# Optimization experiments

Hardware: AMD Instinct MI355X
Metric: run time of the kernel (lower is better)

## Reference

```python
import jax, jax.numpy as jnp
import numpy as np

D_STATE = 16
D_CONV = 4


def layer_norm(x, g, b, eps=1e-5):
    mu = jnp.mean(x, axis=-1, keepdims=True)
    var = jnp.mean(jnp.square(x - mu), axis=-1, keepdims=True)
    return (x - mu) * jax.lax.rsqrt(var + eps) * g + b


def silu(x):
    return x * jax.nn.sigmoid(x)


def mamba(x, in_w, conv_w, conv_b, xproj_w, dt_w, dt_b, Alog, Dp, out_w):
    # x: [B, L, d_model]; in_w: [2*di, d_model]; conv_w: [di, d_conv]
    Bsz, L, _ = x.shape
    di = Dp.shape[0]
    xz = jnp.einsum('bld,ed->ble', x, in_w)          # [B,L,2*di]
    xs, z = jnp.split(xz, 2, axis=-1)
    # causal depthwise conv over L
    xt = xs.transpose(0, 2, 1)                        # [B,di,L]
    xt = jax.lax.conv_general_dilated(
        xt, conv_w[:, None, :], (1,), [(D_CONV - 1, 0)],
        feature_group_count=di, dimension_numbers=('NCH', 'OIH', 'NCH'))
    xs = silu((xt + conv_b[None, :, None]).transpose(0, 2, 1))  # [B,L,di]
    # input-dependent dt, B, C
    dbl = jnp.einsum('bld,ed->ble', xs, xproj_w)      # [B,L,dt_rank+2*ds]
    dt_rank = dt_w.shape[1]
    dt, Bc, Cc = jnp.split(dbl, [dt_rank, dt_rank + D_STATE], axis=-1)
    dt = jax.nn.softplus(jnp.einsum('blr,dr->bld', dt, dt_w) + dt_b)  # [B,L,di]
    A = -jnp.exp(Alog)                                # [di,ds]
    dA = jnp.exp(dt[..., None] * A)                   # [B,L,di,ds]
    dBx = dt[..., None] * Bc[:, :, None, :] * xs[..., None]  # [B,L,di,ds]

    def step(h, inp):
        dA_t, dBx_t, C_t = inp                        # [B,di,ds],[B,di,ds],[B,ds]
        h = dA_t * h + dBx_t
        y = jnp.einsum('bds,bs->bd', h, C_t)
        return h, y

    h0 = jnp.zeros((Bsz, di, D_STATE), x.dtype)
    _, ys = jax.lax.scan(step, h0, (dA.transpose(1, 0, 2, 3),
                                    dBx.transpose(1, 0, 2, 3),
                                    Cc.transpose(1, 0, 2)))
    y = ys.transpose(1, 0, 2) + Dp * xs               # [B,L,di]
    y = y * silu(z)
    return jnp.einsum('bld,od->blo', y, out_w)        # [B,L,d_model]


def _make_mamba_params(key, d_model, scale=0.02):
    di = 2 * d_model
    dt_rank = (d_model + 15) // 16
    ks = jax.random.split(key, 7)
    in_w = jax.random.normal(ks[0], (2 * di, d_model), jnp.float32) * scale
    conv_w = jax.random.normal(ks[1], (di, D_CONV), jnp.float32) * scale
    conv_b = jnp.zeros((di,), jnp.float32)
    xproj_w = jax.random.normal(ks[2], (dt_rank + 2 * D_STATE, di), jnp.float32) * scale
    dt_w = jax.random.normal(ks[3], (di, dt_rank), jnp.float32) * scale
    dt_b = jax.random.uniform(ks[4], (di,), jnp.float32, -5.0, -2.0)
    Alog = jnp.log(jnp.tile(jnp.arange(1, D_STATE + 1, dtype=jnp.float32), (di, 1)))
    Dp = jnp.ones((di,), jnp.float32)
    out_w = jax.random.normal(ks[5], (d_model, di), jnp.float32) * scale
    return in_w, conv_w, conv_b, xproj_w, dt_w, dt_b, Alog, Dp, out_w


def setup_inputs() -> dict:
    key = jax.random.key(0)
    B, L, D = 4, 2048, 1024
    DFF = 4 * D
    ks = jax.random.split(key, 8)
    x = jax.random.normal(ks[0], (B, L, D), jnp.float32)
    m1 = _make_mamba_params(ks[1], D)
    m2 = _make_mamba_params(ks[2], D)
    names1 = ['m1_in_w', 'm1_conv_w', 'm1_conv_b', 'm1_xproj_w', 'm1_dt_w', 'm1_dt_b', 'm1_Alog', 'm1_D', 'm1_out_w']
    names2 = ['m2_in_w', 'm2_conv_w', 'm2_conv_b', 'm2_xproj_w', 'm2_dt_w', 'm2_dt_b', 'm2_Alog', 'm2_D', 'm2_out_w']
    inp = {'x': x}
    inp.update(dict(zip(names1, m1)))
    inp.update(dict(zip(names2, m2)))
    inp['norm_g'] = jnp.ones((D,), jnp.float32)
    inp['norm_b'] = jnp.zeros((D,), jnp.float32)
    inp['ffn_g'] = jnp.ones((D,), jnp.float32)
    inp['ffn_b'] = jnp.zeros((D,), jnp.float32)
    inp['ff1_w'] = jax.random.normal(ks[3], (DFF, D), jnp.float32) * 0.02
    inp['ff1_b'] = jnp.zeros((DFF,), jnp.float32)
    inp['ff2_w'] = jax.random.normal(ks[4], (D, DFF), jnp.float32) * 0.02
    inp['ff2_b'] = jnp.zeros((D,), jnp.float32)
    return inp


def reference(x,
              m1_in_w, m1_conv_w, m1_conv_b, m1_xproj_w, m1_dt_w, m1_dt_b, m1_Alog, m1_D, m1_out_w,
              m2_in_w, m2_conv_w, m2_conv_b, m2_xproj_w, m2_dt_w, m2_dt_b, m2_Alog, m2_D, m2_out_w,
              norm_g, norm_b, ffn_g, ffn_b, ff1_w, ff1_b, ff2_w, ff2_b):
    # BiDirectionalAddBlock (dropout/droppath = identity in eval)
    h = layer_norm(x, norm_g, norm_b)
    fwd = mamba(h, m1_in_w, m1_conv_w, m1_conv_b, m1_xproj_w, m1_dt_w, m1_dt_b, m1_Alog, m1_D, m1_out_w)
    bwd = mamba(h[:, ::-1], m2_in_w, m2_conv_w, m2_conv_b, m2_xproj_w, m2_dt_w, m2_dt_b, m2_Alog, m2_D, m2_out_w)
    block_out = jax.nn.gelu(fwd + bwd + x, approximate=False)  # note: original does NOT flip bwd back
    x = x + block_out
    # FeedForward
    hf = layer_norm(x, ffn_g, ffn_b)
    hf = jax.nn.gelu(jnp.einsum('bld,hd->blh', hf, ff1_w) + ff1_b, approximate=False)
    x = x + jnp.einsum('blh,dh->bld', hf, ff2_w) + ff2_b
    return x
```

## Files before the change

kernel.cpp:

```cpp
#include <hip/hip_runtime.h>
#include <cmath>


namespace {

using u16 = unsigned short;
using uint = unsigned int;

constexpr int kB = 4;
constexpr int kL = 2048;
constexpr int kD = 1024;
constexpr int kDI = 2048;
constexpr int kDFF = 4096;
constexpr int kDS = 16;
constexpr int kDtRank = 64;
constexpr int kNPad = 128;
constexpr int kM = kB * kL;
constexpr int kNCH = 64;

typedef short bf16x8 __attribute__((ext_vector_type(8)));
typedef float f32x4  __attribute__((ext_vector_type(4)));

__device__ __forceinline__ float bf2f(u16 u) {
  union { unsigned int i; float f; } c; c.i = ((unsigned int)u) << 16; return c.f;
}
__device__ __forceinline__ u16 f2bf(float f) {
  union { float f; unsigned int i; } c; c.f = f;
  return (u16)((c.i + 0x7FFFu + ((c.i >> 16) & 1u)) >> 16);
}
__device__ __forceinline__ float geluf(float v) {
  return 0.5f * v * (1.f + erff(v * 0.70710678118654752f));
}
__device__ __forceinline__ float softplusf(float v) {
  return (v > 0.f) ? (v + log1pf(__expf(-v))) : log1pf(__expf(v));
}
__device__ __forceinline__ float siluf(float v) {
  return v / (1.f + __expf(-v));
}
__device__ __forceinline__ float exp2_fast(float v) {
  return __builtin_amdgcn_exp2f(v);
}

__device__ __forceinline__ void async16(const u16* g, u16* l) {
  __builtin_amdgcn_global_load_lds(
      (const __attribute__((address_space(1))) uint*)g,
      (__attribute__((address_space(3))) uint*)l, 16, 0, 0);
}

__global__ __launch_bounds__(256) void ln_kernel(
    const float* __restrict__ x, const float* __restrict__ g,
    const float* __restrict__ b, u16* __restrict__ out) {
  const int row = blockIdx.x;
  const int tid = threadIdx.x;
  const float4 v = ((const float4*)(x + (size_t)row * kD))[tid];
  float s  = v.x + v.y + v.z + v.w;
  float ss = v.x * v.x + v.y * v.y + v.z * v.z + v.w * v.w;
  #pragma unroll
  for (int off = 32; off; off >>= 1) {
    s  += __shfl_xor(s, off);
    ss += __shfl_xor(ss, off);
  }
  __shared__ float ls[4], lss[4];
  const int wid = tid >> 6;
  if ((tid & 63) == 0) { ls[wid] = s; lss[wid] = ss; }
  __syncthreads();
  s  = ls[0] + ls[1] + ls[2] + ls[3];
  ss = lss[0] + lss[1] + lss[2] + lss[3];
  const float mu  = s * (1.f / kD);
  const float inv = rsqrtf(ss * (1.f / kD) - mu * mu + 1e-5f);
  const float4 gg = ((const float4*)g)[tid];
  const float4 bb = ((const float4*)b)[tid];
  ushort4 o;
  o.x = f2bf((v.x - mu) * inv * gg.x + bb.x);
  o.y = f2bf((v.y - mu) * inv * gg.y + bb.y);
  o.z = f2bf((v.z - mu) * inv * gg.z + bb.z);
  o.w = f2bf((v.w - mu) * inv * gg.w + bb.w);
  ((ushort4*)(out + (size_t)row * kD))[tid] = o;
}

__global__ __launch_bounds__(256) void combine_ln_kernel(
    const float* __restrict__ x, float* __restrict__ out,
    const float* __restrict__ g, const float* __restrict__ b,
    u16* __restrict__ h) {
  const int row = blockIdx.x;
  const int tid = threadIdx.x;
  const float4 xv = ((const float4*)(x + (size_t)row * kD))[tid];
  const float4 bv = ((const float4*)(out + (size_t)row * kD))[tid];
  float4 o;
  o.x = xv.x + geluf(bv.x + xv.x);
  o.y = xv.y + geluf(bv.y + xv.y);
  o.z = xv.z + geluf(bv.z + xv.z);
  o.w = xv.w + geluf(bv.w + xv.w);
  ((float4*)(out + (size_t)row * kD))[tid] = o;
  float s  = o.x + o.y + o.z + o.w;
  float ss = o.x * o.x + o.y * o.y + o.z * o.z + o.w * o.w;
  #pragma unroll
  for (int off = 32; off; off >>= 1) {
    s  += __shfl_xor(s, off);
    ss += __shfl_xor(ss, off);
  }
  __shared__ float ls[4], lss[4];
  const int wid = tid >> 6;
  if ((tid & 63) == 0) { ls[wid] = s; lss[wid] = ss; }
  __syncthreads();
  s  = ls[0] + ls[1] + ls[2] + ls[3];
  ss = lss[0] + lss[1] + lss[2] + lss[3];
  const float mu  = s * (1.f / kD);
  const float inv = rsqrtf(ss * (1.f / kD) - mu * mu + 1e-5f);
  const float4 gg = ((const float4*)g)[tid];
  const float4 bb = ((const float4*)b)[tid];
  ushort4 ho;
  ho.x = f2bf((o.x - mu) * inv * gg.x + bb.x);
  ho.y = f2bf((o.y - mu) * inv * gg.y + bb.y);
  ho.z = f2bf((o.z - mu) * inv * gg.z + bb.z);
  ho.w = f2bf((o.w - mu) * inv * gg.w + bb.w);
  ((ushort4*)(h + (size_t)row * kD))[tid] = ho;
}

struct KJob { const float* s; u16* d; int n4; int blk0; int xp; };
struct KJobs { KJob j[10]; };

__global__ __launch_bounds__(256) void cvt_all_kernel(KJobs J) {
  const int bi = blockIdx.x;
  #pragma unroll
  for (int k = 0; k < 10; k++) {
    const KJob job = J.j[k];
    const int nb = (job.n4 + 255) >> 8;
    if (bi >= job.blk0 && bi < job.blk0 + nb) {
      const int i = (bi - job.blk0) * 256 + threadIdx.x;
      if (i < job.n4) {
        ushort4 o = {0, 0, 0, 0};
        bool valid = true;
        if (job.xp) valid = ((i * 4) >> 11) < (kDtRank + 2 * kDS);
        if (valid) {
          const float4 v = ((const float4*)job.s)[i];
          o.x = f2bf(v.x); o.y = f2bf(v.y); o.z = f2bf(v.z); o.w = f2bf(v.w);
        }
        ((ushort4*)job.d)[i] = o;
      }
      return;
    }
  }
}

template <int TILEN, int ACT, bool BIAS, bool ACC, bool OUTBF, bool REV,
          bool AMAP, bool CMAP>
__global__ __launch_bounds__(256) void gemm_mfma(
    const u16* __restrict__ A, int lda,
    const u16* __restrict__ W, int ldw,
    void* __restrict__ Cp, int ldc, int K,
    const float* __restrict__ bias, int seg_len, int row_off) {
  constexpr int MI = (TILEN == 128) ? 4 : 2;
  constexpr int WSTR = TILEN / 32;
  __shared__ __align__(16) u16 As[128][64];
  __shared__ __align__(16) u16 Ws[TILEN][64];
  const int tid  = threadIdx.x;
  const int bm   = blockIdx.x * 128;
  const int bn   = blockIdx.y * TILEN;
  const int lane = tid & 63;
  const int wv   = tid >> 6;
  const int wm   = (TILEN == 128) ? (wv >> 1) * 64 : wv * 32;
  const int wn   = (TILEN == 128) ? (wv & 1) * 64 : 0;
  const int l15  = lane & 15;
  const int quad = lane >> 4;
  const int srow = lane >> 3;
  const int swz  = ((lane & 7) ^ srow) * 8;
  const int jx   = (l15 & 7) * 16;

  int ab = 0, all0 = bm;
  if (AMAP || CMAP) {
    ab = bm / seg_len;
    all0 = bm - ab * seg_len;
  }

  int arowv[4];
  #pragma unroll
  for (int it = 0; it < 4; it++) {
    const int rl = it * 32 + wv * 8 + srow;
    if (AMAP) {
      arowv[it] = REV ? (ab * kL + kL - 1 - row_off - all0 - rl)
                      : (ab * kL + row_off + all0 + rl);
    } else {
      arowv[it] = bm + rl;
    }
  }

  f32x4 acc[MI][4];
  #pragma unroll
  for (int i = 0; i < MI; i++)
    #pragma unroll
    for (int j = 0; j < 4; j++) acc[i][j] = (f32x4){0.f, 0.f, 0.f, 0.f};

  for (int k0 = 0; k0 < K; k0 += 64) {
    #pragma unroll
    for (int it = 0; it < 4; it++) {
      const int rl = it * 32 + wv * 8 + srow;
      async16(A + (size_t)arowv[it] * lda + k0 + swz, &As[it * 32 + wv * 8][0]);
    }
    #pragma unroll
    for (int it = 0; it < WSTR; it++) {
      const int rl = it * 32 + wv * 8 + srow;
      async16(W + (size_t)(bn + rl) * ldw + k0 + swz, &Ws[it * 32 + wv * 8][0]);
    }
    __syncthreads();
    #pragma unroll
    for (int ks = 0; ks < 64; ks += 32) {
      const int cb = ((ks >> 3) + quad) * 16;
      bf16x8 af[MI], wf[4];
      #pragma unroll
      for (int i = 0; i < MI; i++)
        af[i] = *(const bf16x8*)((const char*)&As[wm + i * 16 + l15][0] +
                                 (cb ^ jx));
      #pragma unroll
      for (int j = 0; j < 4; j++)
        wf[j] = *(const bf16x8*)((const char*)&Ws[wn + j * 16 + l15][0] +
                                 (cb ^ jx));
      #pragma unroll
      for (int i = 0; i < MI; i++)
        #pragma unroll
        for (int j = 0; j < 4; j++)
          acc[i][j] = __builtin_amdgcn_mfma_f32_16x16x32_bf16(
              af[i], wf[j], acc[i][j], 0, 0, 0);
    }
    __syncthreads();
  }

  #pragma unroll
  for (int i = 0; i < MI; i++) {
    #pragma unroll
    for (int j = 0; j < 4; j++) {
      const int col = bn + wn + j * 16 + l15;
      #pragma unroll
      for (int r = 0; r < 4; r++) {
        const int rl2 = wm + i * 16 + quad * 4 + r;
        const int crow = CMAP ? (ab * kL + row_off + all0 + rl2) : (bm + rl2);
        float v = acc[i][j][r];
        if (BIAS) v += bias[col];
        if (ACT == 1) v = softplusf(v);
        if (ACT == 2) v = geluf(v);
        if (OUTBF) {
          ((u16*)Cp)[(size_t)crow * ldc + col] = f2bf(v);
        } else {
          float* p = (float*)Cp + (size_t)crow * ldc + col;
          if (ACC) *p = *p + v; else *p = v;
        }
      }
    }
  }
}

__global__ __launch_bounds__(256) void conv_silu_kernel(
    const u16* __restrict__ xz, const float* __restrict__ w,
    const float* __restrict__ cb, u16* __restrict__ xs,
    const u16* __restrict__ tail_in, u16* __restrict__ tail_out,
    int seg_len, int row_off) {
  const int t = blockIdx.x * 256 + threadIdx.x;
  const int c = t & (kDI - 1);
  const int r = t >> 11;
  const int b = r / seg_len;
  const int ll = r - b * seg_len;
  const int tpos = row_off + ll;

  const float xv0 = bf2f(xz[(size_t)r * (2 * kDI) + c]);
  float acc = cb[c] + w[c * 4 + 3] * xv0;
  #pragma unroll
  for (int j = 1; j <= 3; j++) {
    if (tpos - j >= 0) {
      float xp;
      if (ll - j >= 0) {
        xp = bf2f(xz[(size_t)(r - j) * (2 * kDI) + c]);
      } else {
        xp = bf2f(tail_in[(b * 3 + (3 + ll - j)) * kDI + c]);
      }
      acc += w[c * 4 + 3 - j] * xp;
    }
  }
  xs[(size_t)r * kDI + c] = f2bf(siluf(acc));
  if (ll >= seg_len - 3) {
    tail_out[(b * 3 + (ll - (seg_len - 3))) * kDI + c] = f2bf(xv0);
  }
}

__global__ __launch_bounds__(256, 8) void scan_phaseA(
    const u16* __restrict__ dt, const u16* __restrict__ xs,
    const u16* __restrict__ dbl, const float* __restrict__ Alog,
    float* __restrict__ Pbuf, float* __restrict__ Hbuf,
    int Lseg, int Lc) {
  __shared__ float Bls[32][16];
  const int tid = threadIdx.x;
  const int c = blockIdx.x * 256 + tid;
  const int k = blockIdx.y;
  const int b = blockIdx.z;
  const int base = b * Lseg + k * Lc;
  for (int idx = tid; idx < Lc * 16; idx += 256) {
    const int r = idx >> 4, j = idx & 15;
    Bls[r][j] = bf2f(dbl[(size_t)(base + r) * kNPad + kDtRank + j]);
  }
  __syncthreads();
  float Ac[16], h[16];
  float dtsum = 0.f;
  #pragma unroll
  for (int s = 0; s < 16; s++) {
    Ac[s] = -__expf(Alog[c * kDS + s]) * 1.44269504088896f;
    h[s] = 0.f;
  }
  for (int r = 0; r < Lc; r++) {
    const size_t row = (size_t)(base + r);
    const float dtv = bf2f(dt[row * kDI + c]);
    const float dtx = dtv * bf2f(xs[row * kDI + c]);
    dtsum += dtv;
    const float4* Brow = (const float4*)Bls[r];
    #pragma unroll
    for (int s4 = 0; s4 < 4; s4++) {
      const float4 Bv = Brow[s4];
      const float bb[4] = {Bv.x, Bv.y, Bv.z, Bv.w};
      #pragma unroll
      for (int q = 0; q < 4; q++) {
        const int s = s4 * 4 + q;
        const float dA = exp2_fast(dtv * Ac[s]);
        h[s] = dA * h[s] + dtx * bb[q];
      }
    }
  }
  const size_t o = (((size_t)b * kNCH + k) * kDI + c) * 16;
  #pragma unroll
  for (int s4 = 0; s4 < 4; s4++) {
    *(float4*)&Pbuf[o + s4 * 4] =
        make_float4(exp2_fast(Ac[s4 * 4 + 0] * dtsum),
                    exp2_fast(Ac[s4 * 4 + 1] * dtsum),
                    exp2_fast(Ac[s4 * 4 + 2] * dtsum),
                    exp2_fast(Ac[s4 * 4 + 3] * dtsum));
    *(float4*)&Hbuf[o + s4 * 4] =
        make_float4(h[s4 * 4], h[s4 * 4 + 1], h[s4 * 4 + 2], h[s4 * 4 + 3]);
  }
}

__global__ __launch_bounds__(256) void scan_phaseB(
    float* __restrict__ Pbuf, const float* __restrict__ Hbuf,
    float* __restrict__ hstate, int first) {
  const int t = blockIdx.x * 256 + threadIdx.x;
  const int s = t & 15;
  const int c = (t >> 4) & (kDI - 1);
  const int b = t >> 15;
  float cur = first ? 0.f : hstate[t];
  for (int k = 0; k < kNCH; k++) {
    const size_t idx = (((size_t)b * kNCH + k) * kDI + c) * 16 + s;
    const float p = Pbuf[idx];
    const float hl = Hbuf[idx];
    Pbuf[idx] = cur;
    cur = p * cur + hl;
  }
  hstate[t] = cur;
}

__global__ __launch_bounds__(256, 8) void scan_phaseC(
    const u16* __restrict__ dt, u16* __restrict__ xs,
    const u16* __restrict__ dbl, const u16* __restrict__ xz,
    const float* __restrict__ Alog, const float* __restrict__ Dp,
    const float* __restrict__ Pbuf, int Lseg, int Lc) {
  __shared__ float BC[32][32];
  const int tid = threadIdx.x;
  const int c = blockIdx.x * 256 + tid;
  const int k = blockIdx.y;
  const int b = blockIdx.z;
  const int base = b * Lseg + k * Lc;
  for (int idx = tid; idx < Lc * 32; idx += 256) {
    const int r = idx >> 5, j = idx & 31;
    BC[r][j] = bf2f(dbl[(size_t)(base + r) * kNPad + kDtRank + j]);
  }
  __syncthreads();
  float Ac[16], h[16];
  const size_t o = (((size_t)b * kNCH + k) * kDI + c) * 16;
  #pragma unroll
  for (int s4 = 0; s4 < 4; s4++) {
    const float4 hv = *(const float4*)&Pbuf[o + s4 * 4];
    h[s4 * 4 + 0] = hv.x; h[s4 * 4 + 1] = hv.y;
    h[s4 * 4 + 2] = hv.z; h[s4 * 4 + 3] = hv.w;
  }
  #pragma unroll
  for (int s = 0; s < 16; s++)
    Ac[s] = -__expf(Alog[c * kDS + s]) * 1.44269504088896f;
  const float Dv = Dp[c];
  for (int r = 0; r < Lc; r++) {
    const size_t row = (size_t)(base + r);
    const float dtv = bf2f(dt[row * kDI + c]);
    const float xv = bf2f(xs[row * kDI + c]);
    const float dtx = dtv * xv;
    float y = 0.f;
    const float4* Brow = (const float4*)BC[r];
    const float4* Crow = (const float4*)&BC[r][16];
    #pragma unroll
    for (int s4 = 0; s4 < 4; s4++) {
      const float4 Bv = Brow[s4];
      const float4 Cv = Crow[s4];
      const float bb[4] = {Bv.x, Bv.y, Bv.z, Bv.w};
      const float cc[4] = {Cv.x, Cv.y, Cv.z, Cv.w};
      #pragma unroll
      for (int q = 0; q < 4; q++) {
        const int s = s4 * 4 + q;
        const float dA = exp2_fast(dtv * Ac[s]);
        h[s] = dA * h[s] + dtx * bb[q];
        y += h[s] * cc[q];
      }
    }
    const float z = bf2f(xz[row * (2 * kDI) + kDI + c]);
    xs[row * kDI + c] = f2bf((y + Dv * xv) * siluf(z));
  }
}

}

extern "C" void kernel_launch(void* const* d_in, const int* in_sizes, int n_in,
                              void* d_out, int out_size, void* d_ws,
                              size_t ws_size, hipStream_t stream) {
  const float* x = (const float*)d_in[0];
  const float* in_w[2]    = {(const float*)d_in[1],  (const float*)d_in[10]};
  const float* conv_w[2]  = {(const float*)d_in[2],  (const float*)d_in[11]};
  const float* conv_b[2]  = {(const float*)d_in[3],  (const float*)d_in[12]};
  const float* xproj_w[2] = {(const float*)d_in[4],  (const float*)d_in[13]};
  const float* dt_w[2]    = {(const float*)d_in[5],  (const float*)d_in[14]};
  const float* dt_b[2]    = {(const float*)d_in[6],  (const float*)d_in[15]};
  const float* Alog[2]    = {(const float*)d_in[7],  (const float*)d_in[16]};
  const float* Dp[2]      = {(const float*)d_in[8],  (const float*)d_in[17]};
  const float* out_w[2]   = {(const float*)d_in[9],  (const float*)d_in[18]};
  const float* norm_g = (const float*)d_in[19];
  const float* norm_b = (const float*)d_in[20];
  const float* ffn_g  = (const float*)d_in[21];
  const float* ffn_b  = (const float*)d_in[22];
  const float* ff1_w  = (const float*)d_in[23];
  const float* ff1_b  = (const float*)d_in[24];
  const float* ff2_w  = (const float*)d_in[25];
  const float* ff2_b  = (const float*)d_in[26];
  float* out = (float*)d_out;

  constexpr size_t kWCache =
      2 * ((size_t)4096 * kD + (size_t)kD * kDI + (size_t)kNPad * kDI +
           (size_t)kDI * kDtRank) * 2 +
      ((size_t)kDFF * kD + (size_t)kD * kDFF) * 2;
  auto need = [](int nseg) -> size_t {
    const size_t mseg = (size_t)kM / nseg;
    size_t sz = kWCache + 4096;
    sz += (size_t)kM * kD * 2;
    sz += mseg * 4096 * 2;
    sz += mseg * 2048 * 2;
    sz += mseg * 128 * 2;
    sz += mseg * 2048 * 2;
    sz += 2 * (size_t)kB * kNCH * kDI * kDS * 4;
    sz += (size_t)kB * kDI * kDS * 4;
    sz += 2 * (size_t)kB * 3 * kDI * 2;
    sz += 32 * 256;
    return sz;
  };
  int nseg = 1;
  while (nseg <= 16 && need(nseg) > ws_size) nseg *= 2;
  if (nseg > 16) return;
  const int Lseg = kL / nseg;
  const int Mseg = kM / nseg;
  const int Lc = Lseg / kNCH;

  char* base = (char*)d_ws;
  size_t off = 0;
  auto alloc = [&](size_t bytes) {
    char* p = base + off;
    off = (off + bytes + 255) & ~(size_t)255;
    return p;
  };
  u16* w_in[2], *w_out[2], *w_xp[2], *w_dt[2];
  for (int m = 0; m < 2; m++) {
    w_in[m]  = (u16*)alloc((size_t)4096 * kD * 2);
    w_out[m] = (u16*)alloc((size_t)kD * kDI * 2);
    w_xp[m]  = (u16*)alloc((size_t)kNPad * kDI * 2);
    w_dt[m]  = (u16*)alloc((size_t)kDI * kDtRank * 2);
  }
  u16* w_f1 = (u16*)alloc((size_t)kDFF * kD * 2);
  u16* w_f2 = (u16*)alloc((size_t)kD * kDFF * 2);
  u16*   h      = (u16*)alloc((size_t)kM * kD * 2);
  u16*   xz     = (u16*)alloc((size_t)Mseg * 4096 * 2);
  u16*   xs     = (u16*)alloc((size_t)Mseg * 2048 * 2);
  u16*   dbl    = (u16*)alloc((size_t)Mseg * 128 * 2);
  u16*   dtb    = (u16*)alloc((size_t)Mseg * 2048 * 2);
  float* Pbuf   = (float*)alloc((size_t)kB * kNCH * kDI * kDS * 4);
  float* Hbuf   = (float*)alloc((size_t)kB * kNCH * kDI * kDS * 4);
  float* hstate = (float*)alloc((size_t)kB * kDI * kDS * 4);
  u16*   tail0  = (u16*)alloc((size_t)kB * 3 * kDI * 2);
  u16*   tail1  = (u16*)alloc((size_t)kB * 3 * kDI * 2);

  {
    KJobs J;
    int b = 0, ji = 0;
    auto addjob = [&](const float* s, u16* d, int n4, int xp) {
      J.j[ji].s = s; J.j[ji].d = d; J.j[ji].n4 = n4;
      J.j[ji].blk0 = b; J.j[ji].xp = xp;
      b += (n4 + 255) >> 8;
      ji++;
    };
    for (int m = 0; m < 2; m++) {
      addjob(in_w[m],  w_in[m],  (4096 * kD) / 4, 0);
      addjob(out_w[m], w_out[m], (kD * kDI) / 4, 0);
      addjob(xproj_w[m], w_xp[m], (kNPad * kDI) / 4, 1);
      addjob(dt_w[m],  w_dt[m],  (kDI * kDtRank) / 4, 0);
    }
    addjob(ff1_w, w_f1, (kDFF * kD) / 4, 0);
    addjob(ff2_w, w_f2, (kD * kDFF) / 4, 0);
    cvt_all_kernel<<<b, 256, 0, stream>>>(J);
  }

  ln_kernel<<<kM, 256, 0, stream>>>(x, norm_g, norm_b, h);

  for (int m = 0; m < 2; m++) {
    for (int s = 0; s < nseg; s++) {
      const int l0 = s * Lseg;
      u16* tin  = (s & 1) ? tail0 : tail1;
      u16* tout = (s & 1) ? tail1 : tail0;
      if (m == 0)
        gemm_mfma<128, 0, false, false, true, false, true, false>
            <<<dim3(Mseg / 128, 4096 / 128), 256, 0, stream>>>(
                h, kD, w_in[m], kD, xz, 4096, kD, nullptr, Lseg, l0);
      else
        gemm_mfma<128, 0, false, false, true, true, true, false>
            <<<dim3(Mseg / 128, 4096 / 128), 256, 0, stream>>>(
                h, kD, w_in[m], kD, xz, 4096, kD, nullptr, Lseg, l0);
      conv_silu_kernel<<<(Mseg * kDI) / 256, 256, 0, stream>>>(
          xz, conv_w[m], conv_b[m], xs, tin, tout, Lseg, l0);
      gemm_mfma<128, 0, false, false, true, false, false, false>
          <<<dim3(Mseg / 128, 1), 256, 0, stream>>>(
              xs, kDI, w_xp[m], kDI, dbl, kNPad, kDI, nullptr, Lseg, l0);
      gemm_mfma<128, 1, true, false, true, false, false, false>
          <<<dim3(Mseg / 128, kDI / 128), 256, 0, stream>>>(
              dbl, kNPad, w_dt[m], kDtRank, dtb, kDI, kDtRank, dt_b[m],
              Lseg, l0);
      scan_phaseA<<<dim3(kDI / 256, kNCH, kB), 256, 0, stream>>>(
          dtb, xs, dbl, Alog[m], Pbuf, Hbuf, Lseg, Lc);
      scan_phaseB<<<(kB * kDI * kDS) / 256, 256, 0, stream>>>(
          Pbuf, Hbuf, hstate, (s == 0) ? 1 : 0);
      scan_phaseC<<<dim3(kDI / 256, kNCH, kB), 256, 0, stream>>>(
          dtb, xs, dbl, xz, Alog[m], Dp[m], Pbuf, Lseg, Lc);
      if (m == 0)
        gemm_mfma<64, 0, false, false, false, false, false, true>
            <<<dim3(Mseg / 128, kD / 64), 256, 0, stream>>>(
                xs, kDI, w_out[m], kDI, out, kD, kDI, nullptr, Lseg, l0);
      else
        gemm_mfma<64, 0, false, true, false, false, false, true>
            <<<dim3(Mseg / 128, kD / 64), 256, 0, stream>>>(
                xs, kDI, w_out[m], kDI, out, kD, kDI, nullptr, Lseg, l0);
    }
  }

  combine_ln_kernel<<<kM, 256, 0, stream>>>(x, out, ffn_g, ffn_b, h);

  for (int s = 0; s < nseg; s++) {
    const int r0 = s * Mseg;
    gemm_mfma<128, 2, true, false, true, false, true, false>
        <<<dim3(Mseg / 128, kDFF / 128), 256, 0, stream>>>(
            h, kD, w_f1, kD, xz, kDFF, kD, ff1_b, Mseg, r0);
    gemm_mfma<64, 0, true, true, false, false, false, true>
        <<<dim3(Mseg / 128, kD / 64), 256, 0, stream>>>(
            xz, kDFF, w_f2, kDFF, out, kD, kDFF, ff2_b, Mseg, r0);
  }
}
```

Before: 1.371 ms.

## Add triple-buffered 128x256 GEMM kernel for large projections

```diff
diff --git a/kernel.cpp b/kernel.cpp
--- a/kernel.cpp
+++ b/kernel.cpp
@@ -143,24 +143,142 @@
   }
 }
 
-template <int TILEN, int ACT, bool BIAS, bool ACC, bool OUTBF, bool REV,
-          bool AMAP, bool CMAP>
+template <int ACT, bool BIAS, bool ACC, bool OUTBF, bool REV, bool AMAP,
+          bool CMAP>
+__global__ __launch_bounds__(512) void gemm_pipe(
+    const u16* __restrict__ A, int lda,
+    const u16* __restrict__ W, int ldw,
+    void* __restrict__ Cp, int ldc, int K,
+    const float* __restrict__ bias, int seg_len, int row_off) {
+  __shared__ __align__(16) u16 Abuf[3][128][64];
+  __shared__ __align__(16) u16 Bbuf[3][256][64];
+  const int tid  = threadIdx.x;
+  const int bm   = blockIdx.x * 128;
+  const int bn   = blockIdx.y * 256;
+  const int lane = tid & 63;
+  const int w    = tid >> 6;
+  const int wr   = w >> 2;
+  const int wc   = w & 3;
+  const int l15  = lane & 15;
+  const int quad = lane >> 4;
+  const int lrow = lane >> 3;
+  const int swz  = ((lane & 7) ^ lrow) * 8;
+  const int jx   = (l15 & 7) * 16;
+
+  int ab = 0, all0 = bm;
+  if (AMAP || CMAP) { ab = bm / seg_len; all0 = bm - ab * seg_len; }
+
+  int arow[2];
+  #pragma unroll
+  for (int it = 0; it < 2; it++) {
+    const int rl = it * 64 + w * 8 + lrow;
+    arow[it] = AMAP ? (REV ? (ab * kL + kL - 1 - row_off - all0 - rl)
+                           : (ab * kL + row_off + all0 + rl))
+                    : (bm + rl);
+  }
+  int brow[4];
+  #pragma unroll
+  for (int it = 0; it < 4; it++) brow[it] = bn + it * 64 + w * 8 + lrow;
+
+  const int NT = K >> 6;
+
+  f32x4 acc[4][4];
+  #pragma unroll
+  for (int i = 0; i < 4; i++)
+    #pragma unroll
+    for (int j = 0; j < 4; j++) acc[i][j] = (f32x4){0.f, 0.f, 0.f, 0.f};
+
+  auto stage = [&](int bi, int t) {
+    const int k0 = t * 64;
+    #pragma unroll
+    for (int it = 0; it < 2; it++)
+      async16(A + (size_t)arow[it] * lda + k0 + swz,
+              &Abuf[bi][it * 64 + w * 8][0]);
+    #pragma unroll
+    for (int it = 0; it < 4; it++)
+      async16(W + (size_t)brow[it] * ldw + k0 + swz,
+              &Bbuf[bi][it * 64 + w * 8][0]);
+  };
+
+  stage(0, 0);
+  stage(1, 1);
+  asm volatile("s_waitcnt vmcnt(6)\n\ts_barrier" ::: "memory");
+
+  int cur = 0, nxt = 1, nx2 = 2;
+  #pragma unroll 1
+  for (int t = 0; t < NT; t++) {
+    if (t + 2 < NT) stage(nx2, t + 2);
+    bf16x8 af[4][2], wf[4][2];
+    #pragma unroll
+    for (int ks = 0; ks < 2; ks++) {
+      const int cb = (ks * 4 + quad) * 16;
+      #pragma unroll
+      for (int i = 0; i < 4; i++)
+        af[i][ks] = *(const bf16x8*)(
+            (const char*)&Abuf[cur][wr * 64 + i * 16 + l15][0] + (cb ^ jx));
+      #pragma unroll
+      for (int j = 0; j < 4; j++)
+        wf[j][ks] = *(const bf16x8*)(
+            (const char*)&Bbuf[cur][wc * 64 + j * 16 + l15][0] + (cb ^ jx));
+    }
+    __builtin_amdgcn_s_setprio(1);
+    #pragma unroll
+    for (int ks = 0; ks < 2; ks++)
+      #pragma unroll
+      for (int i = 0; i < 4; i++)
+        #pragma unroll
+        for (int j = 0; j < 4; j++)
+          acc[i][j] = __builtin_amdgcn_mfma_f32_16x16x32_bf16(
+              af[i][ks], wf[j][ks], acc[i][j], 0, 0, 0);
+    __builtin_amdgcn_s_setprio(0);
+    if (t + 2 < NT) {
+      asm volatile("s_waitcnt vmcnt(6)\n\ts_barrier" ::: "memory");
+    } else if (t + 2 == NT) {
+      asm volatile("s_waitcnt vmcnt(0)\n\ts_barrier" ::: "memory");
+    }
+    const int tmp = cur; cur = nxt; nxt = nx2; nx2 = tmp;
+  }
+
+  #pragma unroll
+  for (int i = 0; i < 4; i++) {
+    #pragma unroll
+    for (int j = 0; j < 4; j++) {
+      const int col = bn + wc * 64 + j * 16 + l15;
+      #pragma unroll
+      for (int r = 0; r < 4; r++) {
+        const int rl2 = wr * 64 + i * 16 + quad * 4 + r;
+        const int crow = CMAP ? (ab * kL + row_off + all0 + rl2) : (bm + rl2);
+        float v = acc[i][j][r];
+        if (BIAS) v += bias[col];
+        if (ACT == 1) v = softplusf(v);
+        if (ACT == 2) v = geluf(v);
+        if (OUTBF) {
+          ((u16*)Cp)[(size_t)crow * ldc + col] = f2bf(v);
+        } else {
+          float* p = (float*)Cp + (size_t)crow * ldc + col;
+          if (ACC) *p = *p + v; else *p = v;
+        }
+      }
+    }
+  }
+}
+
+template <int ACT, bool BIAS, bool ACC, bool OUTBF, bool REV, bool AMAP,
+          bool CMAP>
 __global__ __launch_bounds__(256) void gemm_mfma(
     const u16* __restrict__ A, int lda,
     const u16* __restrict__ W, int ldw,
     void* __restrict__ Cp, int ldc, int K,
     const float* __restrict__ bias, int seg_len, int row_off) {
-  constexpr int MI = (TILEN == 128) ? 4 : 2;
-  constexpr int WSTR = TILEN / 32;
   __shared__ __align__(16) u16 As[128][64];
-  __shared__ __align__(16) u16 Ws[TILEN][64];
+  __shared__ __align__(16) u16 Ws[128][64];
   const int tid  = threadIdx.x;
   const int bm   = blockIdx.x * 128;
-  const int bn   = blockIdx.y * TILEN;
+  const int bn   = blockIdx.y * 128;
   const int lane = tid & 63;
   const int wv   = tid >> 6;
-  const int wm   = (TILEN == 128) ? (wv >> 1) * 64 : wv * 32;
-  const int wn   = (TILEN == 128) ? (wv & 1) * 64 : 0;
+  const int wm   = (wv >> 1) * 64;
+  const int wn   = (wv & 1) * 64;
   const int l15  = lane & 15;
   const int quad = lane >> 4;
   const int srow = lane >> 3;
@@ -185,9 +303,9 @@
     }
   }
 
-  f32x4 acc[MI][4];
-  #pragma unroll
-  for (int i = 0; i < MI; i++)
+  f32x4 acc[4][4];
+  #pragma unroll
+  for (int i = 0; i < 4; i++)
     #pragma unroll
     for (int j = 0; j < 4; j++) acc[i][j] = (f32x4){0.f, 0.f, 0.f, 0.f};
 
@@ -196,19 +314,15 @@
     for (int it = 0; it < 4; it++) {
       const int rl = it * 32 + wv * 8 + srow;
       async16(A + (size_t)arowv[it] * lda + k0 + swz, &As[it * 32 + wv * 8][0]);
-    }
-    #pragma unroll
-    for (int it = 0; it < WSTR; it++) {
-      const int rl = it * 32 + wv * 8 + srow;
       async16(W + (size_t)(bn + rl) * ldw + k0 + swz, &Ws[it * 32 + wv * 8][0]);
     }
     __syncthreads();
     #pragma unroll
     for (int ks = 0; ks < 64; ks += 32) {
       const int cb = ((ks >> 3) + quad) * 16;
-      bf16x8 af[MI], wf[4];
-      #pragma unroll
-      for (int i = 0; i < MI; i++)
+      bf16x8 af[4], wf[4];
+      #pragma unroll
+      for (int i = 0; i < 4; i++)
         af[i] = *(const bf16x8*)((const char*)&As[wm + i * 16 + l15][0] +
                                  (cb ^ jx));
       #pragma unroll
@@ -216,7 +330,7 @@
         wf[j] = *(const bf16x8*)((const char*)&Ws[wn + j * 16 + l15][0] +
                                  (cb ^ jx));
       #pragma unroll
-      for (int i = 0; i < MI; i++)
+      for (int i = 0; i < 4; i++)
         #pragma unroll
         for (int j = 0; j < 4; j++)
           acc[i][j] = __builtin_amdgcn_mfma_f32_16x16x32_bf16(
@@ -226,7 +340,7 @@
   }
 
   #pragma unroll
-  for (int i = 0; i < MI; i++) {
+  for (int i = 0; i < 4; i++) {
     #pragma unroll
     for (int j = 0; j < 4; j++) {
       const int col = bn + wn + j * 16 + l15;
@@ -513,19 +627,19 @@
       u16* tin  = (s & 1) ? tail0 : tail1;
       u16* tout = (s & 1) ? tail1 : tail0;
       if (m == 0)
-        gemm_mfma<128, 0, false, false, true, false, true, false>
-            <<<dim3(Mseg / 128, 4096 / 128), 256, 0, stream>>>(
+        gemm_pipe<0, false, false, true, false, true, false>
+            <<<dim3(Mseg / 128, 4096 / 256), 512, 0, stream>>>(
                 h, kD, w_in[m], kD, xz, 4096, kD, nullptr, Lseg, l0);
       else
-        gemm_mfma<128, 0, false, false, true, true, true, false>
-            <<<dim3(Mseg / 128, 4096 / 128), 256, 0, stream>>>(
+        gemm_pipe<0, false, false, true, true, true, false>
+            <<<dim3(Mseg / 128, 4096 / 256), 512, 0, stream>>>(
                 h, kD, w_in[m], kD, xz, 4096, kD, nullptr, Lseg, l0);
       conv_silu_kernel<<<(Mseg * kDI) / 256, 256, 0, stream>>>(
           xz, conv_w[m], conv_b[m], xs, tin, tout, Lseg, l0);
-      gemm_mfma<128, 0, false, false, true, false, false, false>
+      gemm_mfma<0, false, false, true, false, false, false>
           <<<dim3(Mseg / 128, 1), 256, 0, stream>>>(
               xs, kDI, w_xp[m], kDI, dbl, kNPad, kDI, nullptr, Lseg, l0);
-      gemm_mfma<128, 1, true, false, true, false, false, false>
+      gemm_mfma<1, true, false, true, false, false, false>
           <<<dim3(Mseg / 128, kDI / 128), 256, 0, stream>>>(
               dbl, kNPad, w_dt[m], kDtRank, dtb, kDI, kDtRank, dt_b[m],
               Lseg, l0);
@@ -536,12 +650,12 @@
       scan_phaseC<<<dim3(kDI / 256, kNCH, kB), 256, 0, stream>>>(
           dtb, xs, dbl, xz, Alog[m], Dp[m], Pbuf, Lseg, Lc);
       if (m == 0)
-        gemm_mfma<64, 0, false, false, false, false, false, true>
-            <<<dim3(Mseg / 128, kD / 64), 256, 0, stream>>>(
+        gemm_pipe<0, false, false, false, false, false, true>
+            <<<dim3(Mseg / 128, kD / 256), 512, 0, stream>>>(
                 xs, kDI, w_out[m], kDI, out, kD, kDI, nullptr, Lseg, l0);
       else
-        gemm_mfma<64, 0, false, true, false, false, false, true>
-            <<<dim3(Mseg / 128, kD / 64), 256, 0, stream>>>(
+        gemm_pipe<0, false, true, false, false, false, true>
+            <<<dim3(Mseg / 128, kD / 256), 512, 0, stream>>>(
                 xs, kDI, w_out[m], kDI, out, kD, kDI, nullptr, Lseg, l0);
     }
   }
@@ -550,11 +664,11 @@
 
   for (int s = 0; s < nseg; s++) {
     const int r0 = s * Mseg;
-    gemm_mfma<128, 2, true, false, true, false, true, false>
-        <<<dim3(Mseg / 128, kDFF / 128), 256, 0, stream>>>(
+    gemm_pipe<2, true, false, true, false, true, false>
+        <<<dim3(Mseg / 128, kDFF / 256), 512, 0, stream>>>(
             h, kD, w_f1, kD, xz, kDFF, kD, ff1_b, Mseg, r0);
-    gemm_mfma<64, 0, true, true, false, false, false, true>
-        <<<dim3(Mseg / 128, kD / 64), 256, 0, stream>>>(
+    gemm_pipe<0, true, true, false, false, false, true>
+        <<<dim3(Mseg / 128, kD / 256), 512, 0, stream>>>(
             xz, kDFF, w_f2, kDFF, out, kD, kDFF, ff2_b, Mseg, r0);
   }
 }
```

New measurement: 1.480 ms. 1.08x slower.
